# Kernel tuning notes

Measured on AMD Instinct MI355X. Metric: run time of the kernel, lower is better.

## Reference

```python
import jax, jax.numpy as jnp
import numpy as np

N = 100000       # nodes
E = 1600000      # edges (avg degree 16)
C_IN = 128
C_OUT = 64
C_HID = 2 * C_OUT  # 128, matches GCNEncoder's 2*out_channels hidden width


def setup_inputs() -> dict:
    key = jax.random.key(0)
    k1, k2, k3, k4 = jax.random.split(key, 4)
    x = jax.random.normal(k1, (N, C_IN), dtype=jnp.float32)
    edge_index = jax.random.randint(k2, (2, E), 0, N, dtype=jnp.int64)
    # Glorot-ish scale for the linear weights (PyG GCNConv uses glorot init)
    W1 = jax.random.normal(k3, (C_IN, C_HID), dtype=jnp.float32) / np.sqrt(C_IN)
    b1 = jnp.zeros((C_HID,), dtype=jnp.float32)
    W2 = jax.random.normal(k4, (C_HID, C_OUT), dtype=jnp.float32) / np.sqrt(C_HID)
    b2 = jnp.zeros((C_OUT,), dtype=jnp.float32)
    return {"x": x, "edge_index": edge_index, "W1": W1, "b1": b1, "W2": W2, "b2": b2}


def _gcn_conv(x, src, dst, norm_e, self_norm, W, b):
    # GCNConv: out = D^{-1/2} (A + I) D^{-1/2} (x @ W) + b
    h = x @ W                                   # [N, C'] transform first (cheaper)
    msg = h[src] * norm_e[:, None]              # [E, C'] gather + edge normalization
    agg = jax.ops.segment_sum(msg, dst, num_segments=N)  # scatter-add over targets
    return agg + self_norm[:, None] * h + b     # self-loop term + bias


def reference(x, edge_index, W1, b1, W2, b2):
    src, dst = edge_index[0], edge_index[1]
    # degrees on A + I (self-loops added), identical for both layers
    deg = jax.ops.segment_sum(jnp.ones((E,), jnp.float32), dst, num_segments=N) + 1.0
    dinv = jax.lax.rsqrt(deg)                   # deg >= 1, no zero-guard needed
    norm_e = dinv[src] * dinv[dst]              # [E]
    self_norm = dinv * dinv                     # [N]

    h = _gcn_conv(x, src, dst, norm_e, self_norm, W1, b1)
    h = jax.nn.relu(h)
    return _gcn_conv(h, src, dst, norm_e, self_norm, W2, b2)
```

## Files before the change

### kernel.cpp

```cpp
#include <hip/hip_runtime.h>
#include <hip/hip_fp16.h>

#define NN   100000
#define NE   1600000
#define CIN  128
#define CHID 128
#define COUT 64

#define NPB  256
#define NB   391
#define NBLK 128
#define CHUNK ((NE + NBLK - 1) / NBLK)
#define BPAD 2048

typedef _Float16 f16x8 __attribute__((ext_vector_type(8)));
typedef float    f32x4 __attribute__((ext_vector_type(4)));

#define NTILE 782
#define GGRID 512

__global__ void k_zrow(__half* __restrict__ g1, __half* __restrict__ g2) {
  int t = threadIdx.x;
  if (t < 128) g1[(size_t)NN * CHID + t] = __float2half(0.f);
  if (t < 64)  g2[(size_t)NN * COUT + t] = __float2half(0.f);
}

__global__ __launch_bounds__(512) void k_passA(const int* __restrict__ dst,
                                               int* __restrict__ tab) {
  __shared__ int hist[NB];
  int tid = threadIdx.x;
  for (int t = tid; t < NB; t += 512) hist[t] = 0;
  __syncthreads();
  int i0 = blockIdx.x * CHUNK;
  int i1 = min(i0 + CHUNK, NE);
  for (int i = i0 + tid; i < i1; i += 512)
    atomicAdd(&hist[((unsigned)dst[i]) >> 8], 1);
  __syncthreads();
  for (int t = tid; t < NB; t += 512)
    tab[t * NBLK + blockIdx.x] = hist[t];
}

__global__ __launch_bounds__(512) void k_bscan(const int* __restrict__ tab,
                                               int* __restrict__ bb) {
  __shared__ int s[512];
  int t = threadIdx.x;
  int v = 0;
  if (t < NB) {
    const int* row = tab + t * NBLK;
#pragma unroll 8
    for (int k = 0; k < NBLK; k++) v += row[k];
  }
  s[t] = v;
  __syncthreads();
  for (int off = 1; off < 512; off <<= 1) {
    int u = (t >= off) ? s[t - off] : 0;
    __syncthreads();
    s[t] += u;
    __syncthreads();
  }
  if (t < NB) bb[t] = s[t] - v;
  if (t == 0) bb[NB] = NE;
}

__global__ __launch_bounds__(128) void k_tabscan(int* __restrict__ tab,
                                                 const int* __restrict__ bb) {
  __shared__ int s[128];
  int b = blockIdx.x, t = threadIdx.x;
  int v = tab[b * NBLK + t];
  s[t] = v;
  __syncthreads();
  for (int off = 1; off < 128; off <<= 1) {
    int u = (t >= off) ? s[t - off] : 0;
    __syncthreads();
    s[t] += u;
    __syncthreads();
  }
  tab[b * NBLK + t] = bb[b] + s[t] - v;
}

__global__ __launch_bounds__(512) void k_passB(const int* __restrict__ src,
                                               const int* __restrict__ dst,
                                               const int* __restrict__ tab,
                                               int* __restrict__ barr) {
  __shared__ int cur[NB];
  int tid = threadIdx.x;
  for (int t = tid; t < NB; t += 512) cur[t] = tab[t * NBLK + blockIdx.x];
  __syncthreads();
  int i0 = blockIdx.x * CHUNK;
  int i1 = min(i0 + CHUNK, NE);
  for (int i = i0 + tid; i < i1; i += 512) {
    int d = dst[i];
    unsigned b = ((unsigned)d) >> 8;
    int p = atomicAdd(&cur[b], 1);
    barr[p] = (src[i] << 8) | (d & 255);
  }
}

__global__ __launch_bounds__(256) void k_l2(const int* __restrict__ barr,
                                            const int* __restrict__ bb,
                                            int* __restrict__ csr,
                                            int* __restrict__ rs,
                                            int* __restrict__ re,
                                            float* __restrict__ dinv) {
  __shared__ int lcnt[NPB];
  __shared__ int lcur[NPB];
  int b = blockIdx.x, t = threadIdx.x;
  int e0 = bb[b], e1 = bb[b + 1];
  lcnt[t] = 0;
  __syncthreads();
  for (int i = e0 + t; i < e1; i += 256) atomicAdd(&lcnt[barr[i] & 255], 1);
  __syncthreads();
  int v = lcnt[t];
  int pv = (v + 7) & ~7;
  lcur[t] = pv;
  __syncthreads();
  for (int off = 1; off < 256; off <<= 1) {
    int u = (t >= off) ? lcur[t - off] : 0;
    __syncthreads();
    lcur[t] += u;
    __syncthreads();
  }
  int pex = lcur[t] - pv;
  int start = e0 + b * BPAD + pex;
  int g = b * NPB + t;
  if (g < NN) {
    rs[g] = start;
    re[g] = start + pv;
    dinv[g] = rsqrtf((float)v + 1.0f);
  }
  __syncthreads();
  lcur[t] = start;
  for (int k = v; k < pv; k++) csr[start + k] = NN;
  __syncthreads();
  for (int i = e0 + t; i < e1; i += 256) {
    int w = barr[i];
    int p = atomicAdd(&lcur[w & 255], 1);
    csr[p] = ((unsigned)w) >> 8;
  }
}

__global__ __launch_bounds__(256, 2) void k_gemm1(const float* __restrict__ X,
                                                  const float* __restrict__ W,
                                                  const float* __restrict__ dinv,
                                                  __half* __restrict__ G) {
  __shared__ _Float16 Wt[128][128];
  int tid = threadIdx.x;
  for (int i = tid; i < 128 * 32; i += 256) {
    int k = i >> 5, c4 = (i & 31) << 2;
    float4 v = ((const float4*)W)[i];
    Wt[c4 + 0][k] = (_Float16)v.x;
    Wt[c4 + 1][k] = (_Float16)v.y;
    Wt[c4 + 2][k] = (_Float16)v.z;
    Wt[c4 + 3][k] = (_Float16)v.w;
  }
  __syncthreads();
  int wv = tid >> 6, lane = tid & 63;
  int l15 = lane & 15, g = lane >> 4;

  f16x8 wf[8][4];
#pragma unroll
  for (int cf = 0; cf < 8; cf++)
#pragma unroll
    for (int ks = 0; ks < 4; ks++)
      wf[cf][ks] = *(const f16x8*)&Wt[cf * 16 + l15][ks * 32 + g * 8];

  for (int t = blockIdx.x; t < NTILE; t += GGRID) {
    int rowbase = t * 128 + wv * 32;
    f32x4 acc[2][8];
#pragma unroll
    for (int i = 0; i < 2; i++)
#pragma unroll
      for (int j = 0; j < 8; j++) acc[i][j] = (f32x4){0.f, 0.f, 0.f, 0.f};

    int r0 = min(rowbase + l15, NN - 1);
    int r1 = min(rowbase + 16 + l15, NN - 1);
    const float* p0 = X + (size_t)r0 * CIN + g * 8;
    const float* p1 = X + (size_t)r1 * CIN + g * 8;

    float4 u0a = *(const float4*)p0, u0b = *(const float4*)(p0 + 4);
    float4 u1a = *(const float4*)p1, u1b = *(const float4*)(p1 + 4);

#pragma unroll
    for (int ks = 0; ks < 4; ks++) {
      f16x8 xa, xb;
      xa[0] = (_Float16)u0a.x; xa[1] = (_Float16)u0a.y;
      xa[2] = (_Float16)u0a.z; xa[3] = (_Float16)u0a.w;
      xa[4] = (_Float16)u0b.x; xa[5] = (_Float16)u0b.y;
      xa[6] = (_Float16)u0b.z; xa[7] = (_Float16)u0b.w;
      xb[0] = (_Float16)u1a.x; xb[1] = (_Float16)u1a.y;
      xb[2] = (_Float16)u1a.z; xb[3] = (_Float16)u1a.w;
      xb[4] = (_Float16)u1b.x; xb[5] = (_Float16)u1b.y;
      xb[6] = (_Float16)u1b.z; xb[7] = (_Float16)u1b.w;
      if (ks < 3) {
        int o = (ks + 1) * 32;
        u0a = *(const float4*)(p0 + o); u0b = *(const float4*)(p0 + o + 4);
        u1a = *(const float4*)(p1 + o); u1b = *(const float4*)(p1 + o + 4);
      }
#pragma unroll
      for (int cf = 0; cf < 8; cf++) {
        acc[0][cf] = __builtin_amdgcn_mfma_f32_16x16x32_f16(wf[cf][ks], xa, acc[0][cf], 0, 0, 0);
        acc[1][cf] = __builtin_amdgcn_mfma_f32_16x16x32_f16(wf[cf][ks], xb, acc[1][cf], 0, 0, 0);
      }
    }

#pragma unroll
    for (int rf = 0; rf < 2; rf++) {
      int row = rowbase + rf * 16 + l15;
      if (row < NN) {
        float dn = dinv[row];
#pragma unroll
        for (int cf = 0; cf < 8; cf++) {
          int col = cf * 16 + g * 4;
          __half2 h0 = __half2(__float2half(dn * acc[rf][cf][0]),
                               __float2half(dn * acc[rf][cf][1]));
          __half2 h1 = __half2(__float2half(dn * acc[rf][cf][2]),
                               __float2half(dn * acc[rf][cf][3]));
          uint2 s;
          s.x = *(unsigned*)&h0;
          s.y = *(unsigned*)&h1;
          *(uint2*)(G + (size_t)row * CHID + col) = s;
        }
      }
    }
  }
}

__global__ __launch_bounds__(256, 2) void k_gemm2(const __half* __restrict__ X,
                                                  const float* __restrict__ W,
                                                  const float* __restrict__ dinv,
                                                  __half* __restrict__ G) {
  __shared__ _Float16 Wt[64][128];
  int tid = threadIdx.x;
  for (int i = tid; i < 128 * 16; i += 256) {
    int k = i >> 4, c4 = (i & 15) << 2;
    float4 v = ((const float4*)W)[i];
    Wt[c4 + 0][k] = (_Float16)v.x;
    Wt[c4 + 1][k] = (_Float16)v.y;
    Wt[c4 + 2][k] = (_Float16)v.z;
    Wt[c4 + 3][k] = (_Float16)v.w;
  }
  __syncthreads();
  int wv = tid >> 6, lane = tid & 63;
  int l15 = lane & 15, g = lane >> 4;

  f16x8 wf[4][4];
#pragma unroll
  for (int cf = 0; cf < 4; cf++)
#pragma unroll
    for (int ks = 0; ks < 4; ks++)
      wf[cf][ks] = *(const f16x8*)&Wt[cf * 16 + l15][ks * 32 + g * 8];

  for (int t = blockIdx.x; t < NTILE; t += GGRID) {
    int rowbase = t * 128 + wv * 32;
    f32x4 acc[2][4];
#pragma unroll
    for (int i = 0; i < 2; i++)
#pragma unroll
      for (int j = 0; j < 4; j++) acc[i][j] = (f32x4){0.f, 0.f, 0.f, 0.f};

    int r0 = min(rowbase + l15, NN - 1);
    int r1 = min(rowbase + 16 + l15, NN - 1);
    const _Float16* p0 = (const _Float16*)X + (size_t)r0 * CHID + g * 8;
    const _Float16* p1 = (const _Float16*)X + (size_t)r1 * CHID + g * 8;

    f16x8 xa = *(const f16x8*)p0;
    f16x8 xb = *(const f16x8*)p1;

#pragma unroll
    for (int ks = 0; ks < 4; ks++) {
      f16x8 ca = xa, cb = xb;
      if (ks < 3) {
        int o = (ks + 1) * 32;
        xa = *(const f16x8*)(p0 + o);
        xb = *(const f16x8*)(p1 + o);
      }
#pragma unroll
      for (int cf = 0; cf < 4; cf++) {
        acc[0][cf] = __builtin_amdgcn_mfma_f32_16x16x32_f16(wf[cf][ks], ca, acc[0][cf], 0, 0, 0);
        acc[1][cf] = __builtin_amdgcn_mfma_f32_16x16x32_f16(wf[cf][ks], cb, acc[1][cf], 0, 0, 0);
      }
    }

#pragma unroll
    for (int rf = 0; rf < 2; rf++) {
      int row = rowbase + rf * 16 + l15;
      if (row < NN) {
        float dn = dinv[row];
#pragma unroll
        for (int cf = 0; cf < 4; cf++) {
          int col = cf * 16 + g * 4;
          __half2 h0 = __half2(__float2half(dn * acc[rf][cf][0]),
                               __float2half(dn * acc[rf][cf][1]));
          __half2 h1 = __half2(__float2half(dn * acc[rf][cf][2]),
                               __float2half(dn * acc[rf][cf][3]));
          uint2 s;
          s.x = *(unsigned*)&h0;
          s.y = *(unsigned*)&h1;
          *(uint2*)(G + (size_t)row * COUT + col) = s;
        }
      }
    }
  }
}

#define ACC8(A, V)                                                  \
  {                                                                 \
    float2 f;                                                       \
    f = __half22float2(*(__half2*)&(V).x); A[0] += f.x; A[1] += f.y; \
    f = __half22float2(*(__half2*)&(V).y); A[2] += f.x; A[3] += f.y; \
    f = __half22float2(*(__half2*)&(V).z); A[4] += f.x; A[5] += f.y; \
    f = __half22float2(*(__half2*)&(V).w); A[6] += f.x; A[7] += f.y; \
  }

__global__ __launch_bounds__(256) void k_agg1(const __half* __restrict__ g,
                                              const int* __restrict__ rs,
                                              const int* __restrict__ re,
                                              const float* __restrict__ dinv,
                                              const int* __restrict__ csr,
                                              const float* __restrict__ b,
                                              __half* __restrict__ o) {
  int wid = (blockIdx.x * blockDim.x + threadIdx.x) >> 6;
  int lane = threadIdx.x & 63;
  if (wid >= NN) return;
  int q = lane >> 4, ql = lane & 15;
  const uint4* gp = (const uint4*)g;

  float aA[8] = {0.f, 0.f, 0.f, 0.f, 0.f, 0.f, 0.f, 0.f};
  float aB[8] = {0.f, 0.f, 0.f, 0.f, 0.f, 0.f, 0.f, 0.f};

  if (q == 0) {
    uint4 v = gp[(size_t)wid * 16 + ql];
    ACC8(aA, v);
  }

  int i0 = rs[wid], i1 = re[wid];
  for (int i = i0; i < i1; i += 8) {
    int sA = csr[i + q];
    int sB = csr[i + 4 + q];
    uint4 vA = gp[(size_t)sA * 16 + ql];
    uint4 vB = gp[(size_t)sB * 16 + ql];
    ACC8(aA, vA);
    ACC8(aB, vB);
  }

  float r[8];
#pragma unroll
  for (int c = 0; c < 8; c++) {
    float t = aA[c] + aB[c];
    t += __shfl_xor(t, 16);
    t += __shfl_xor(t, 32);
    r[c] = t;
  }
  if (q == 0) {
    float dn = dinv[wid];
    float4 b0 = *(const float4*)(b + 8 * ql);
    float4 b1 = *(const float4*)(b + 8 * ql + 4);
    __half2 h[4];
    h[0] = __half2(__float2half(fmaxf(fmaf(dn, r[0], b0.x), 0.f)),
                   __float2half(fmaxf(fmaf(dn, r[1], b0.y), 0.f)));
    h[1] = __half2(__float2half(fmaxf(fmaf(dn, r[2], b0.z), 0.f)),
                   __float2half(fmaxf(fmaf(dn, r[3], b0.w), 0.f)));
    h[2] = __half2(__float2half(fmaxf(fmaf(dn, r[4], b1.x), 0.f)),
                   __float2half(fmaxf(fmaf(dn, r[5], b1.y), 0.f)));
    h[3] = __half2(__float2half(fmaxf(fmaf(dn, r[6], b1.z), 0.f)),
                   __float2half(fmaxf(fmaf(dn, r[7], b1.w), 0.f)));
    *(uint4*)(o + (size_t)wid * CHID + 8 * ql) = *(uint4*)h;
  }
}

__global__ __launch_bounds__(256) void k_agg2(const __half* __restrict__ g,
                                              const int* __restrict__ rs,
                                              const int* __restrict__ re,
                                              const float* __restrict__ dinv,
                                              const int* __restrict__ csr,
                                              const float* __restrict__ b,
                                              float* __restrict__ o) {
  int wid = (blockIdx.x * blockDim.x + threadIdx.x) >> 6;
  int lane = threadIdx.x & 63;
  if (wid >= NN) return;
  int g8 = lane >> 3, gl = lane & 7;
  const uint4* gp = (const uint4*)g;

  float aA[8] = {0.f, 0.f, 0.f, 0.f, 0.f, 0.f, 0.f, 0.f};

  if (g8 == 0) {
    uint4 v = gp[(size_t)wid * 8 + gl];
    ACC8(aA, v);
  }

  int i0 = rs[wid], i1 = re[wid];
  for (int i = i0; i < i1; i += 8) {
    int s = csr[i + g8];
    uint4 v = gp[(size_t)s * 8 + gl];
    ACC8(aA, v);
  }

  float r[8];
#pragma unroll
  for (int c = 0; c < 8; c++) {
    float t = aA[c];
    t += __shfl_xor(t, 8);
    t += __shfl_xor(t, 16);
    t += __shfl_xor(t, 32);
    r[c] = t;
  }
  if (g8 == 0) {
    float dn = dinv[wid];
    float4 b0 = *(const float4*)(b + 8 * gl);
    float4 b1 = *(const float4*)(b + 8 * gl + 4);
    float4 o0 = make_float4(fmaf(dn, r[0], b0.x), fmaf(dn, r[1], b0.y),
                            fmaf(dn, r[2], b0.z), fmaf(dn, r[3], b0.w));
    float4 o1v = make_float4(fmaf(dn, r[4], b1.x), fmaf(dn, r[5], b1.y),
                             fmaf(dn, r[6], b1.z), fmaf(dn, r[7], b1.w));
    *(float4*)(o + (size_t)wid * COUT + 8 * gl) = o0;
    *(float4*)(o + (size_t)wid * COUT + 8 * gl + 4) = o1v;
  }
}


extern "C" void kernel_launch(void* const* d_in, const int* in_sizes, int n_in,
                              void* d_out, int out_size, void* d_ws, size_t ws_size,
                              hipStream_t stream) {
  const float* x  = (const float*)d_in[0];
  const int*   ei = (const int*)d_in[1];
  const float* W1 = (const float*)d_in[2];
  const float* b1 = (const float*)d_in[3];
  const float* W2 = (const float*)d_in[4];
  const float* b2 = (const float*)d_in[5];
  float* out = (float*)d_out;

  const int* esrc = ei;
  const int* edst = ei + NE;

  char* p = (char*)d_ws;
  __half* g1 = (__half*)p;    p += (size_t)(NN + 1) * CHID * 2;
  __half* o1 = (__half*)p;    p += (size_t)NN * CHID * 2;
  __half* g2 = (__half*)p;    p += (size_t)(NN + 1) * COUT * 2;
  int* rs  = (int*)p;         p += (size_t)NN * 4;
  int* re  = (int*)p;         p += (size_t)NN * 4;
  float* dinv = (float*)p;    p += (size_t)NN * 4;
  int* tab = (int*)p;         p += (size_t)NB * NBLK * 4;
  int* bb  = (int*)p;         p += (size_t)(NB + 1) * 4;
  int* barr = (int*)p;        p += (size_t)NE * 4;
  int* csr = (int*)p;         p += (size_t)(NE + NB * BPAD) * 4;

  hipLaunchKernelGGL(k_zrow, dim3(1), dim3(128), 0, stream, g1, g2);

  hipLaunchKernelGGL(k_passA, dim3(NBLK), dim3(512), 0, stream, edst, tab);
  hipLaunchKernelGGL(k_bscan, dim3(1), dim3(512), 0, stream, tab, bb);
  hipLaunchKernelGGL(k_tabscan, dim3(NB), dim3(128), 0, stream, tab, bb);
  hipLaunchKernelGGL(k_passB, dim3(NBLK), dim3(512), 0, stream, esrc, edst, tab, barr);
  hipLaunchKernelGGL(k_l2, dim3(NB), dim3(256), 0, stream, barr, bb, csr, rs, re, dinv);

  hipLaunchKernelGGL(k_gemm1, dim3(GGRID), dim3(256), 0, stream, x, W1, dinv, g1);
  hipLaunchKernelGGL(k_agg1, dim3((NN + 3) / 4), dim3(256), 0, stream, g1, rs, re, dinv, csr, b1, o1);

  hipLaunchKernelGGL(k_gemm2, dim3(GGRID), dim3(256), 0, stream, o1, W2, dinv, g2);
  hipLaunchKernelGGL(k_agg2, dim3((NN + 3) / 4), dim3(256), 0, stream, g2, rs, re, dinv, csr, b2, out);
}
```

Baseline: 224.3 us.

## Merge graph-build passes with first GEMM and move source normalization into aggregation

The first GEMM no longer scales rows by dinv, so it can run in the same launch as the edge-bucketing pass (passB), using a block-index split. The per-source dinv factor moves into the layer-1 aggregation loop as an extra gather. The zero-row init is folded into k_l2 and the two scans are merged into one single-block kernel with a sequential per-row prefix. NBLK is doubled. Together these cut kernel launches and let the GEMM overlap with the CSR construction, at the cost of an extra dinv gather per edge in agg1 and a serial scan loop in one block.

```diff
diff --git a/kernel.cpp b/kernel.cpp
--- a/kernel.cpp
+++ b/kernel.cpp
@@ -9,7 +9,7 @@
 
 #define NPB  256
 #define NB   391
-#define NBLK 128
+#define NBLK 256
 #define CHUNK ((NE + NBLK - 1) / NBLK)
 #define BPAD 2048
 
@@ -18,12 +18,6 @@
 
 #define NTILE 782
 #define GGRID 512
-
-__global__ void k_zrow(__half* __restrict__ g1, __half* __restrict__ g2) {
-  int t = threadIdx.x;
-  if (t < 128) g1[(size_t)NN * CHID + t] = __float2half(0.f);
-  if (t < 64)  g2[(size_t)NN * COUT + t] = __float2half(0.f);
-}
 
 __global__ __launch_bounds__(512) void k_passA(const int* __restrict__ dst,
                                                int* __restrict__ tab) {
@@ -40,8 +34,8 @@
     tab[t * NBLK + blockIdx.x] = hist[t];
 }
 
-__global__ __launch_bounds__(512) void k_bscan(const int* __restrict__ tab,
-                                               int* __restrict__ bb) {
+__global__ __launch_bounds__(512) void k_scan(int* __restrict__ tab,
+                                              int* __restrict__ bb) {
   __shared__ int s[512];
   int t = threadIdx.x;
   int v = 0;
@@ -58,93 +52,50 @@
     s[t] += u;
     __syncthreads();
   }
-  if (t < NB) bb[t] = s[t] - v;
+  int base = s[t] - v;
+  if (t < NB) bb[t] = base;
   if (t == 0) bb[NB] = NE;
-}
-
-__global__ __launch_bounds__(128) void k_tabscan(int* __restrict__ tab,
-                                                 const int* __restrict__ bb) {
-  __shared__ int s[128];
-  int b = blockIdx.x, t = threadIdx.x;
-  int v = tab[b * NBLK + t];
-  s[t] = v;
-  __syncthreads();
-  for (int off = 1; off < 128; off <<= 1) {
-    int u = (t >= off) ? s[t - off] : 0;
-    __syncthreads();
-    s[t] += u;
-    __syncthreads();
-  }
-  tab[b * NBLK + t] = bb[b] + s[t] - v;
-}
-
-__global__ __launch_bounds__(512) void k_passB(const int* __restrict__ src,
-                                               const int* __restrict__ dst,
-                                               const int* __restrict__ tab,
-                                               int* __restrict__ barr) {
+  if (t < NB) {
+    int run = base;
+    int* row = tab + t * NBLK;
+    for (int k = 0; k < NBLK; k += 4) {
+      int4 c = *(int4*)(row + k);
+      int4 w;
+      w.x = run; run += c.x;
+      w.y = run; run += c.y;
+      w.z = run; run += c.z;
+      w.w = run; run += c.w;
+      *(int4*)(row + k) = w;
+    }
+  }
+}
+
+__global__ __launch_bounds__(256, 2) void k_pbg1(const int* __restrict__ src,
+                                                 const int* __restrict__ dst,
+                                                 const int* __restrict__ tab,
+                                                 int* __restrict__ barr,
+                                                 const float* __restrict__ X,
+                                                 const float* __restrict__ W,
+                                                 __half* __restrict__ G) {
+  __shared__ _Float16 Wt[128][128];
   __shared__ int cur[NB];
   int tid = threadIdx.x;
-  for (int t = tid; t < NB; t += 512) cur[t] = tab[t * NBLK + blockIdx.x];
-  __syncthreads();
-  int i0 = blockIdx.x * CHUNK;
-  int i1 = min(i0 + CHUNK, NE);
-  for (int i = i0 + tid; i < i1; i += 512) {
-    int d = dst[i];
-    unsigned b = ((unsigned)d) >> 8;
-    int p = atomicAdd(&cur[b], 1);
-    barr[p] = (src[i] << 8) | (d & 255);
-  }
-}
-
-__global__ __launch_bounds__(256) void k_l2(const int* __restrict__ barr,
-                                            const int* __restrict__ bb,
-                                            int* __restrict__ csr,
-                                            int* __restrict__ rs,
-                                            int* __restrict__ re,
-                                            float* __restrict__ dinv) {
-  __shared__ int lcnt[NPB];
-  __shared__ int lcur[NPB];
-  int b = blockIdx.x, t = threadIdx.x;
-  int e0 = bb[b], e1 = bb[b + 1];
-  lcnt[t] = 0;
-  __syncthreads();
-  for (int i = e0 + t; i < e1; i += 256) atomicAdd(&lcnt[barr[i] & 255], 1);
-  __syncthreads();
-  int v = lcnt[t];
-  int pv = (v + 7) & ~7;
-  lcur[t] = pv;
-  __syncthreads();
-  for (int off = 1; off < 256; off <<= 1) {
-    int u = (t >= off) ? lcur[t - off] : 0;
+  int bid = blockIdx.x;
+
+  if (bid < NBLK) {
+    for (int t = tid; t < NB; t += 256) cur[t] = tab[t * NBLK + bid];
     __syncthreads();
-    lcur[t] += u;
-    __syncthreads();
-  }
-  int pex = lcur[t] - pv;
-  int start = e0 + b * BPAD + pex;
-  int g = b * NPB + t;
-  if (g < NN) {
-    rs[g] = start;
-    re[g] = start + pv;
-    dinv[g] = rsqrtf((float)v + 1.0f);
-  }
-  __syncthreads();
-  lcur[t] = start;
-  for (int k = v; k < pv; k++) csr[start + k] = NN;
-  __syncthreads();
-  for (int i = e0 + t; i < e1; i += 256) {
-    int w = barr[i];
-    int p = atomicAdd(&lcur[w & 255], 1);
-    csr[p] = ((unsigned)w) >> 8;
-  }
-}
-
-__global__ __launch_bounds__(256, 2) void k_gemm1(const float* __restrict__ X,
-                                                  const float* __restrict__ W,
-                                                  const float* __restrict__ dinv,
-                                                  __half* __restrict__ G) {
-  __shared__ _Float16 Wt[128][128];
-  int tid = threadIdx.x;
+    int i0 = bid * CHUNK;
+    int i1 = min(i0 + CHUNK, NE);
+    for (int i = i0 + tid; i < i1; i += 256) {
+      int d = dst[i];
+      unsigned b = ((unsigned)d) >> 8;
+      int p = atomicAdd(&cur[b], 1);
+      barr[p] = (src[i] << 8) | (d & 255);
+    }
+    return;
+  }
+
   for (int i = tid; i < 128 * 32; i += 256) {
     int k = i >> 5, c4 = (i & 31) << 2;
     float4 v = ((const float4*)W)[i];
@@ -164,7 +115,7 @@
     for (int ks = 0; ks < 4; ks++)
       wf[cf][ks] = *(const f16x8*)&Wt[cf * 16 + l15][ks * 32 + g * 8];
 
-  for (int t = blockIdx.x; t < NTILE; t += GGRID) {
+  for (int t = bid - NBLK; t < NTILE; t += GGRID) {
     int rowbase = t * 128 + wv * 32;
     f32x4 acc[2][8];
 #pragma unroll
@@ -207,14 +158,13 @@
     for (int rf = 0; rf < 2; rf++) {
       int row = rowbase + rf * 16 + l15;
       if (row < NN) {
-        float dn = dinv[row];
 #pragma unroll
         for (int cf = 0; cf < 8; cf++) {
           int col = cf * 16 + g * 4;
-          __half2 h0 = __half2(__float2half(dn * acc[rf][cf][0]),
-                               __float2half(dn * acc[rf][cf][1]));
-          __half2 h1 = __half2(__float2half(dn * acc[rf][cf][2]),
-                               __float2half(dn * acc[rf][cf][3]));
+          __half2 h0 = __half2(__float2half(acc[rf][cf][0]),
+                               __float2half(acc[rf][cf][1]));
+          __half2 h1 = __half2(__float2half(acc[rf][cf][2]),
+                               __float2half(acc[rf][cf][3]));
           uint2 s;
           s.x = *(unsigned*)&h0;
           s.y = *(unsigned*)&h1;
@@ -222,6 +172,56 @@
         }
       }
     }
+  }
+}
+
+__global__ __launch_bounds__(256) void k_l2(const int* __restrict__ barr,
+                                            const int* __restrict__ bb,
+                                            int* __restrict__ csr,
+                                            int* __restrict__ rs,
+                                            int* __restrict__ re,
+                                            float* __restrict__ dinv,
+                                            __half* __restrict__ g1,
+                                            __half* __restrict__ g2) {
+  __shared__ int lcnt[NPB];
+  __shared__ int lcur[NPB];
+  int b = blockIdx.x, t = threadIdx.x;
+  if (b == 0) {
+    if (t < 128) g1[(size_t)NN * CHID + t] = __float2half(0.f);
+    if (t < 64)  g2[(size_t)NN * COUT + t] = __float2half(0.f);
+    if (t == 0)  dinv[NN] = 0.f;
+  }
+  int e0 = bb[b], e1 = bb[b + 1];
+  lcnt[t] = 0;
+  __syncthreads();
+  for (int i = e0 + t; i < e1; i += 256) atomicAdd(&lcnt[barr[i] & 255], 1);
+  __syncthreads();
+  int v = lcnt[t];
+  int pv = (v + 7) & ~7;
+  lcur[t] = pv;
+  __syncthreads();
+  for (int off = 1; off < 256; off <<= 1) {
+    int u = (t >= off) ? lcur[t - off] : 0;
+    __syncthreads();
+    lcur[t] += u;
+    __syncthreads();
+  }
+  int pex = lcur[t] - pv;
+  int start = e0 + b * BPAD + pex;
+  int g = b * NPB + t;
+  if (g < NN) {
+    rs[g] = start;
+    re[g] = start + pv;
+    dinv[g] = rsqrtf((float)v + 1.0f);
+  }
+  __syncthreads();
+  lcur[t] = start;
+  for (int k = v; k < pv; k++) csr[start + k] = NN;
+  __syncthreads();
+  for (int i = e0 + t; i < e1; i += 256) {
+    int w = barr[i];
+    int p = atomicAdd(&lcur[w & 255], 1);
+    csr[p] = ((unsigned)w) >> 8;
   }
 }
 
@@ -303,6 +303,15 @@
   }
 }
 
+#define ACC8F(A, V, D)                                                        \
+  {                                                                           \
+    float2 f;                                                                 \
+    f = __half22float2(*(__half2*)&(V).x); A[0] = fmaf(D, f.x, A[0]); A[1] = fmaf(D, f.y, A[1]); \
+    f = __half22float2(*(__half2*)&(V).y); A[2] = fmaf(D, f.x, A[2]); A[3] = fmaf(D, f.y, A[3]); \
+    f = __half22float2(*(__half2*)&(V).z); A[4] = fmaf(D, f.x, A[4]); A[5] = fmaf(D, f.y, A[5]); \
+    f = __half22float2(*(__half2*)&(V).w); A[6] = fmaf(D, f.x, A[6]); A[7] = fmaf(D, f.y, A[7]); \
+  }
+
 #define ACC8(A, V)                                                  \
   {                                                                 \
     float2 f;                                                       \
@@ -328,19 +337,22 @@
   float aA[8] = {0.f, 0.f, 0.f, 0.f, 0.f, 0.f, 0.f, 0.f};
   float aB[8] = {0.f, 0.f, 0.f, 0.f, 0.f, 0.f, 0.f, 0.f};
 
+  float dnw = dinv[wid];
   if (q == 0) {
     uint4 v = gp[(size_t)wid * 16 + ql];
-    ACC8(aA, v);
+    ACC8F(aA, v, dnw);
   }
 
   int i0 = rs[wid], i1 = re[wid];
   for (int i = i0; i < i1; i += 8) {
     int sA = csr[i + q];
     int sB = csr[i + 4 + q];
+    float dA = dinv[sA];
+    float dB = dinv[sB];
     uint4 vA = gp[(size_t)sA * 16 + ql];
     uint4 vB = gp[(size_t)sB * 16 + ql];
-    ACC8(aA, vA);
-    ACC8(aB, vB);
+    ACC8F(aA, vA, dA);
+    ACC8F(aB, vB, dB);
   }
 
   float r[8];
@@ -352,18 +364,17 @@
     r[c] = t;
   }
   if (q == 0) {
-    float dn = dinv[wid];
     float4 b0 = *(const float4*)(b + 8 * ql);
     float4 b1 = *(const float4*)(b + 8 * ql + 4);
     __half2 h[4];
-    h[0] = __half2(__float2half(fmaxf(fmaf(dn, r[0], b0.x), 0.f)),
-                   __float2half(fmaxf(fmaf(dn, r[1], b0.y), 0.f)));
-    h[1] = __half2(__float2half(fmaxf(fmaf(dn, r[2], b0.z), 0.f)),
-                   __float2half(fmaxf(fmaf(dn, r[3], b0.w), 0.f)));
-    h[2] = __half2(__float2half(fmaxf(fmaf(dn, r[4], b1.x), 0.f)),
-                   __float2half(fmaxf(fmaf(dn, r[5], b1.y), 0.f)));
-    h[3] = __half2(__float2half(fmaxf(fmaf(dn, r[6], b1.z), 0.f)),
-                   __float2half(fmaxf(fmaf(dn, r[7], b1.w), 0.f)));
+    h[0] = __half2(__float2half(fmaxf(fmaf(dnw, r[0], b0.x), 0.f)),
+                   __float2half(fmaxf(fmaf(dnw, r[1], b0.y), 0.f)));
+    h[1] = __half2(__float2half(fmaxf(fmaf(dnw, r[2], b0.z), 0.f)),
+                   __float2half(fmaxf(fmaf(dnw, r[3], b0.w), 0.f)));
+    h[2] = __half2(__float2half(fmaxf(fmaf(dnw, r[4], b1.x), 0.f)),
+                   __float2half(fmaxf(fmaf(dnw, r[5], b1.y), 0.f)));
+    h[3] = __half2(__float2half(fmaxf(fmaf(dnw, r[6], b1.z), 0.f)),
+                   __float2half(fmaxf(fmaf(dnw, r[7], b1.w), 0.f)));
     *(uint4*)(o + (size_t)wid * CHID + 8 * ql) = *(uint4*)h;
   }
 }
@@ -438,23 +449,23 @@
   __half* g2 = (__half*)p;    p += (size_t)(NN + 1) * COUT * 2;
   int* rs  = (int*)p;         p += (size_t)NN * 4;
   int* re  = (int*)p;         p += (size_t)NN * 4;
-  float* dinv = (float*)p;    p += (size_t)NN * 4;
+  float* dinv = (float*)p;    p += (size_t)(NN + 1) * 4;
   int* tab = (int*)p;         p += (size_t)NB * NBLK * 4;
   int* bb  = (int*)p;         p += (size_t)(NB + 1) * 4;
   int* barr = (int*)p;        p += (size_t)NE * 4;
   int* csr = (int*)p;         p += (size_t)(NE + NB * BPAD) * 4;
 
-  hipLaunchKernelGGL(k_zrow, dim3(1), dim3(128), 0, stream, g1, g2);
-
   hipLaunchKernelGGL(k_passA, dim3(NBLK), dim3(512), 0, stream, edst, tab);
-  hipLaunchKernelGGL(k_bscan, dim3(1), dim3(512), 0, stream, tab, bb);
-  hipLaunchKernelGGL(k_tabscan, dim3(NB), dim3(128), 0, stream, tab, bb);
-  hipLaunchKernelGGL(k_passB, dim3(NBLK), dim3(512), 0, stream, esrc, edst, tab, barr);
-  hipLaunchKernelGGL(k_l2, dim3(NB), dim3(256), 0, stream, barr, bb, csr, rs, re, dinv);
-
-  hipLaunchKernelGGL(k_gemm1, dim3(GGRID), dim3(256), 0, stream, x, W1, dinv, g1);
-  hipLaunchKernelGGL(k_agg1, dim3((NN + 3) / 4), dim3(256), 0, stream, g1, rs, re, dinv, csr, b1, o1);
+  hipLaunchKernelGGL(k_scan, dim3(1), dim3(512), 0, stream, tab, bb);
+  hipLaunchKernelGGL(k_pbg1, dim3(NBLK + GGRID), dim3(256), 0, stream,
+                     esrc, edst, tab, barr, x, W1, g1);
+  hipLaunchKernelGGL(k_l2, dim3(NB), dim3(256), 0, stream, barr, bb, csr, rs, re,
+                     dinv, g1, g2);
+
+  hipLaunchKernelGGL(k_agg1, dim3((NN + 3) / 4), dim3(256), 0, stream,
+                     g1, rs, re, dinv, csr, b1, o1);
 
   hipLaunchKernelGGL(k_gemm2, dim3(GGRID), dim3(256), 0, stream, o1, W2, dinv, g2);
-  hipLaunchKernelGGL(k_agg2, dim3((NN + 3) / 4), dim3(256), 0, stream, g2, rs, re, dinv, csr, b2, out);
-}
+  hipLaunchKernelGGL(k_agg2, dim3((NN + 3) / 4), dim3(256), 0, stream,
+                     g2, rs, re, dinv, csr, b2, out);
+}
```

Result: slower. 248.9 us (+11.0%).
